# Kernel optimization log

Measured on AMD Instinct MI355X. Metric: run time of the kernel, lower is better.

Reference implementation:

```python
import jax, jax.numpy as jnp
import numpy as np

N_HEADS = 8
NUM_GROUPS = 2
HEAD_DIM = 256
ROPE_DIM = 64
IDIM = 2048
GROUP_SIZE = N_HEADS // NUM_GROUPS  # 4
ODIM = N_HEADS * HEAD_DIM           # 2048
N_KV = NUM_GROUPS * HEAD_DIM        # 512
EPS = 1e-6


def rms_norm(x, gamma):
    # normalize over last dim (head_dim)
    var = jnp.mean(jnp.square(x), axis=-1, keepdims=True)
    return x * jax.lax.rsqrt(var + EPS) * gamma


def rotate_half(x):
    x1, x2 = jnp.split(x, 2, axis=-1)
    return jnp.concatenate([-x2, x1], axis=-1)


def apply_rope(x, cos, sin):
    # x: (..., L, rope_dim); cos/sin: (L, rope_dim) broadcast
    return x * cos + rotate_half(x) * sin


def setup_inputs() -> dict:
    key = jax.random.key(0)
    ks = jax.random.split(key, 10)
    B, L = 1, 4096
    x = jax.random.normal(ks[0], (B, L, IDIM), dtype=jnp.float32)
    # rope angles
    inv_freq = 1.0 / (10000.0 ** (jnp.arange(0, ROPE_DIM, 2, dtype=jnp.float32) / ROPE_DIM))
    t = jnp.arange(L, dtype=jnp.float32)
    freqs = jnp.outer(t, inv_freq)                      # (L, rope_dim/2)
    emb = jnp.concatenate([freqs, freqs], axis=-1)      # (L, rope_dim)
    cos = jnp.cos(emb)
    sin = jnp.sin(emb)
    # causal mask: True = masked out
    mask = jnp.triu(jnp.ones((L, L), dtype=bool), k=1)
    s = 0.02
    wq = jax.random.normal(ks[1], (IDIM, ODIM * 2), dtype=jnp.float32) * s
    wk = jax.random.normal(ks[2], (IDIM, N_KV), dtype=jnp.float32) * s
    wv = jax.random.normal(ks[3], (IDIM, N_KV), dtype=jnp.float32) * s
    wo = jax.random.normal(ks[4], (ODIM, IDIM), dtype=jnp.float32) * s
    q_gamma = jnp.ones((HEAD_DIM,), dtype=jnp.float32)
    k_gamma = jnp.ones((HEAD_DIM,), dtype=jnp.float32)
    return {"x": x, "cos": cos, "sin": sin, "mask": mask,
            "wq": wq, "wk": wk, "wv": wv, "wo": wo,
            "q_gamma": q_gamma, "k_gamma": k_gamma}


def reference(x, cos, sin, mask, wq, wk, wv, wo, q_gamma, k_gamma):
    b, L, _ = x.shape
    scale = HEAD_DIM ** -0.5
    # query + output gate
    q_raw = (x @ wq).reshape(b, L, N_HEADS, 2 * HEAD_DIM)
    q, gate = jnp.split(q_raw, 2, axis=-1)
    gate = gate.reshape(b, L, ODIM)
    q = jnp.transpose(q, (0, 2, 1, 3))                  # (b, h, L, d)
    # grouped K/V
    k = (x @ wk).reshape(b, L, NUM_GROUPS, HEAD_DIM).transpose(0, 2, 1, 3)  # (b, g, L, d)
    v = (x @ wv).reshape(b, L, NUM_GROUPS, HEAD_DIM).transpose(0, 2, 1, 3)
    # QK RMSNorm
    q = rms_norm(q, q_gamma)
    k = rms_norm(k, k_gamma)
    # partial RoPE on first ROPE_DIM dims
    q = jnp.concatenate([apply_rope(q[..., :ROPE_DIM], cos, sin), q[..., ROPE_DIM:]], axis=-1)
    k = jnp.concatenate([apply_rope(k[..., :ROPE_DIM], cos, sin), k[..., ROPE_DIM:]], axis=-1)
    # GQA without materializing repeated K/V: head h = g*GROUP_SIZE + s
    qg = q.reshape(b, NUM_GROUPS, GROUP_SIZE, L, HEAD_DIM)
    dots = jnp.einsum('bgsid,bgjd->bgsij', qg, k) * scale
    dots = jnp.where(mask, -jnp.inf, dots)
    attn = jax.nn.softmax(dots, axis=-1)
    out = jnp.einsum('bgsij,bgjd->bgsid', attn, v)      # (b, g, gs, L, d)
    out = out.reshape(b, N_HEADS, L, HEAD_DIM).transpose(0, 2, 1, 3).reshape(b, L, ODIM)
    out = out * jax.nn.sigmoid(gate)
    return out @ wo
```

## Files before the change

### kernel.cpp

```cpp
#include <hip/hip_runtime.h>
#include <hip/hip_bf16.h>
#include <math.h>

typedef __bf16 bf16_t;
typedef __bf16 bf16x4 __attribute__((ext_vector_type(4)));
typedef __bf16 bf16x8 __attribute__((ext_vector_type(8)));
typedef float  f32x4  __attribute__((ext_vector_type(4)));
typedef float  f32x16 __attribute__((ext_vector_type(16)));
typedef unsigned int u32x4 __attribute__((ext_vector_type(4)));

typedef const __attribute__((address_space(1))) void* gas_ptr;
typedef __attribute__((address_space(3))) void* las_ptr;

#define RD_ 64
#define QKVS 5120

__global__ __launch_bounds__(256) void cvt_f32_bf16(const float* __restrict__ in,
                                                    bf16_t* __restrict__ out) {
  int i = (blockIdx.x * 256 + threadIdx.x) * 4;
  float4 v = *(const float4*)&in[i];
  bf16x4 w;
  w[0] = (bf16_t)v.x; w[1] = (bf16_t)v.y; w[2] = (bf16_t)v.z; w[3] = (bf16_t)v.w;
  *(bf16x4*)&out[i] = w;
}

__global__ __launch_bounds__(256) void transpose_cvt(const float* __restrict__ in,
                                                     bf16_t* __restrict__ out,
                                                     int R, int C) {
  __shared__ bf16_t t[32][33];
  int tx = threadIdx.x & 31, ty = threadIdx.x >> 5;
  int c0 = blockIdx.x * 32, r0 = blockIdx.y * 32;
#pragma unroll
  for (int i = 0; i < 4; i++)
    t[ty + 8 * i][tx] = (bf16_t)in[(size_t)(r0 + ty + 8 * i) * C + c0 + tx];
  __syncthreads();
#pragma unroll
  for (int i = 0; i < 4; i++)
    out[(size_t)(c0 + ty + 8 * i) * R + r0 + tx] = t[tx][ty + 8 * i];
}

__global__ __launch_bounds__(256) void transpose_bf16(const bf16_t* __restrict__ in,
                                                      bf16_t* __restrict__ out,
                                                      int R, int C) {
  __shared__ bf16_t t[32][33];
  int tx = threadIdx.x & 31, ty = threadIdx.x >> 5;
  int c0 = blockIdx.x * 32, r0 = blockIdx.y * 32;
#pragma unroll
  for (int i = 0; i < 4; i++)
    t[ty + 8 * i][tx] = in[(size_t)(r0 + ty + 8 * i) * C + c0 + tx];
  __syncthreads();
#pragma unroll
  for (int i = 0; i < 4; i++)
    out[(size_t)(c0 + ty + 8 * i) * R + r0 + tx] = t[tx][ty + 8 * i];
}

#define GM 128
#define GN 128
#define GK 32

template <typename OutT>
__global__ __launch_bounds__(256) void gemm_bt(const bf16_t* __restrict__ A,
                                               const bf16_t* __restrict__ Bt,
                                               OutT* __restrict__ C,
                                               int M, int N, int K) {
  __shared__ bf16_t As[GM * GK];
  __shared__ bf16_t Bs[GN * GK];
  int tid  = threadIdx.x;
  int lane = tid & 63, wave = tid >> 6;
  int wm = (wave & 1) * 64, wn = (wave >> 1) * 64;
  int bm = blockIdx.x * GM, bn = blockIdx.y * GN;
  int qd = lane >> 4, lr = lane & 15;

  f32x4 acc[4][4] = {};

  int srow = wave * 16 + (lane >> 2);
  int scol = (lane & 3) * 8;
  const bf16_t* ga0 = A  + (size_t)(bm + srow) * K + scol;
  const bf16_t* ga1 = A  + (size_t)(bm + 64 + srow) * K + scol;
  const bf16_t* gb0 = Bt + (size_t)(bn + srow) * K + scol;
  const bf16_t* gb1 = Bt + (size_t)(bn + 64 + srow) * K + scol;
  las_ptr lA0 = (las_ptr)(As + wave * 512);
  las_ptr lA1 = (las_ptr)(As + 64 * 32 + wave * 512);
  las_ptr lB0 = (las_ptr)(Bs + wave * 512);
  las_ptr lB1 = (las_ptr)(Bs + 64 * 32 + wave * 512);

  for (int k0 = 0; k0 < K; k0 += GK) {
    __syncthreads();
    __builtin_amdgcn_global_load_lds((gas_ptr)(ga0 + k0), lA0, 16, 0, 0);
    __builtin_amdgcn_global_load_lds((gas_ptr)(ga1 + k0), lA1, 16, 0, 0);
    __builtin_amdgcn_global_load_lds((gas_ptr)(gb0 + k0), lB0, 16, 0, 0);
    __builtin_amdgcn_global_load_lds((gas_ptr)(gb1 + k0), lB1, 16, 0, 0);
    __syncthreads();

    bf16x8 af[4], bfr[4];
#pragma unroll
    for (int t = 0; t < 4; t++) {
      af[t]  = *(const bf16x8*)&As[(wm + t * 16 + lr) * GK + qd * 8];
      bfr[t] = *(const bf16x8*)&Bs[(wn + t * 16 + lr) * GK + qd * 8];
    }
#pragma unroll
    for (int mt = 0; mt < 4; mt++)
#pragma unroll
      for (int nt = 0; nt < 4; nt++)
        acc[mt][nt] = __builtin_amdgcn_mfma_f32_16x16x32_bf16(af[mt], bfr[nt], acc[mt][nt], 0, 0, 0);
  }

#pragma unroll
  for (int mt = 0; mt < 4; mt++) {
    int rb = bm + wm + mt * 16 + qd * 4;
#pragma unroll
    for (int nt = 0; nt < 4; nt++) {
      int cc = bn + wn + nt * 16 + lr;
#pragma unroll
      for (int r = 0; r < 4; r++)
        C[(size_t)(rb + r) * N + cc] = (OutT)acc[mt][nt][r];
    }
  }
}

template <int NHEADS, int HSTRIDE, int RSTRIDE>
__global__ __launch_bounds__(256) void norm_rope(const bf16_t* __restrict__ in,
                                                 bf16_t* __restrict__ out,
                                                 const float* __restrict__ cosv,
                                                 const float* __restrict__ sinv,
                                                 const float* __restrict__ gamma) {
  int lane = threadIdx.x & 63;
  int idx  = blockIdx.x * 4 + (threadIdx.x >> 6);
  int l = idx / NHEADS, h = idx % NHEADS;
  size_t base = (size_t)l * RSTRIDE + (size_t)h * HSTRIDE;
  int d0 = lane * 4;

  bf16x4 raw = *(const bf16x4*)&in[base + d0];
  float x[4];
#pragma unroll
  for (int i = 0; i < 4; i++) x[i] = (float)raw[i];
  float ss = x[0] * x[0] + x[1] * x[1] + x[2] * x[2] + x[3] * x[3];
#pragma unroll
  for (int off = 32; off >= 1; off >>= 1) ss += __shfl_xor(ss, off);
  float inv = 1.0f / sqrtf(ss * (1.0f / 256.0f) + 1e-6f);

  float4 gr = *(const float4*)&gamma[d0];
  float n[4];
#pragma unroll
  for (int i = 0; i < 4; i++) n[i] = x[i] * inv * ((const float*)&gr)[i];

  float p[4];
#pragma unroll
  for (int i = 0; i < 4; i++) p[i] = __shfl_xor(n[i], 8);
  float o[4];
#pragma unroll
  for (int i = 0; i < 4; i++) o[i] = n[i];
  if (lane < 16) {
    float4 cr = *(const float4*)&cosv[(size_t)l * RD_ + d0];
    float4 sr = *(const float4*)&sinv[(size_t)l * RD_ + d0];
#pragma unroll
    for (int i = 0; i < 4; i++) {
      float rh = (lane < 8) ? -p[i] : p[i];
      o[i] = n[i] * ((const float*)&cr)[i] + rh * ((const float*)&sr)[i];
    }
  }
  bf16x4 w;
#pragma unroll
  for (int i = 0; i < 4; i++) w[i] = (bf16_t)o[i];
  *(bf16x4*)&out[base + d0] = w;
}

__global__ __launch_bounds__(256, 2) void attn_mfma(const bf16_t* __restrict__ qraw,
                                                    const bf16_t* __restrict__ kn,
                                                    const bf16_t* __restrict__ vt,
                                                    bf16_t* __restrict__ outg,
                                                    float* __restrict__ pO,
                                                    float* __restrict__ pL) {
  __shared__ __align__(16) bf16_t ks[2][32 * 256];
  __shared__ __align__(16) bf16_t vs[2][256 * 32];
  int tid = threadIdx.x, lane = tid & 63, wave = tid >> 6;
  int m = lane & 31, hi = lane >> 5;
  int b = blockIdx.x;
  int h = b & 7, g = h >> 2, i = b >> 3;

  int qb, tile0, nt; bool fin = false;
  if (i < 16) { qb = 31 - i; tile0 = 0; nt = 64; }
  else {
    int u = (i - 16) >> 1;
    if (((i - 16) & 1) == 0) { qb = 15 - u; tile0 = 0; nt = 4 * qb + 4; fin = true; }
    else                     { qb = 31 - u; tile0 = 64; nt = 4 * qb + 4 - 64; }
  }

  int qrow0 = qb * 128 + wave * 32;
  int qg = qrow0 + m;
  int qmax = qrow0 + 31;

  bf16x8 qf[16];
  {
    const bf16_t* qp = qraw + (size_t)(qrow0 + m) * QKVS + h * 512 + hi * 8;
#pragma unroll
    for (int kb = 0; kb < 16; kb++) qf[kb] = *(const bf16x8*)(qp + kb * 16);
  }

  int xk = m & 7;
  int kofs[4];
#pragma unroll
  for (int bb = 0; bb < 4; bb++)
    kofs[bb] = m * 256 + ((bb ^ (xk >> 1)) * 2 + (hi ^ (xk & 1))) * 8;
  int swv = (m ^ (m >> 2)) & 3;
  int vofs[2];
#pragma unroll
  for (int k2 = 0; k2 < 2; k2++)
    vofs[k2] = m * 32 + (((k2 * 2 + hi) ^ swv) * 8);

  const bf16_t* ksrc = kn + (size_t)(wave * 2 + hi) * QKVS + g * 256
                          + (size_t)((m ^ ((wave * 2 + hi) & 7)) * 8);
  int swsrc = ((lane >> 2) ^ (lane >> 4)) & 3;
  const bf16_t* vsrc = vt + (size_t)(g * 256 + wave * 16 + (lane >> 2)) * 4096
                          + (size_t)(((lane & 3) ^ swsrc) * 8);

  f32x16 o[8] = {};
  float ladd = 0.0f;

#define STAGE(buf, j0)                                                                      \
  do {                                                                                      \
    bf16_t* kd = &ks[buf][0] + wave * 512;                                                  \
    bf16_t* vd = &vs[buf][0] + wave * 512;                                                  \
    _Pragma("unroll")                                                                       \
    for (int s = 0; s < 4; s++)                                                             \
      __builtin_amdgcn_global_load_lds((gas_ptr)(ksrc + (size_t)(j0) * QKVS + s * 8 * QKVS),\
                                       (las_ptr)(kd + s * 2048), 16, 0, 0);                 \
    _Pragma("unroll")                                                                       \
    for (int s = 0; s < 4; s++)                                                             \
      __builtin_amdgcn_global_load_lds((gas_ptr)(vsrc + (size_t)(j0) + (size_t)s * 262144), \
                                       (las_ptr)(vd + s * 2048), 16, 0, 0);                 \
  } while (0)

  STAGE(0, tile0 * 32);
  asm volatile("s_waitcnt vmcnt(0)" ::: "memory");
  __syncthreads();

  for (int t = 0; t < nt; t++) {
    int cur = t & 1;
    if (t + 1 < nt) STAGE(cur ^ 1, (tile0 + t + 1) * 32);
    int j0 = (tile0 + t) * 32;
    if (j0 <= qmax) {
      f32x16 sa = {};
#pragma unroll
      for (int kb = 0; kb < 16; kb++) {
        bf16x8 kf = *(const bf16x8*)&ks[cur][kofs[kb & 3] + (kb >> 2) * 64];
        sa = __builtin_amdgcn_mfma_f32_32x32x16_bf16(kf, qf[kb], sa, 0, 0, 0);
      }

      bool diag = (j0 + 31 > qrow0);
#pragma unroll
      for (int k2 = 0; k2 < 2; k2++) {
        float pp[8];
#pragma unroll
        for (int r = 0; r < 8; r++) {
          int rr = k2 * 8 + r;
          float e = __expf(sa[rr] * 0.0625f - 20.0f);
          if (diag) {
            int jr = j0 + (rr & 3) + 8 * (rr >> 2) + 4 * hi;
            if (jr > qg) e = 0.0f;
          }
          pp[r] = e;
        }
        unsigned a0, b0, a1, b1;
        asm("v_cvt_pk_bf16_f32 %0, %1, %2" : "=v"(a0) : "v"(pp[0]), "v"(pp[1]));
        asm("v_cvt_pk_bf16_f32 %0, %1, %2" : "=v"(b0) : "v"(pp[4]), "v"(pp[5]));
        asm("v_cvt_pk_bf16_f32 %0, %1, %2" : "=v"(a1) : "v"(pp[2]), "v"(pp[3]));
        asm("v_cvt_pk_bf16_f32 %0, %1, %2" : "=v"(b1) : "v"(pp[6]), "v"(pp[7]));
        asm("v_permlane32_swap_b32 %0, %1" : "+v"(a0), "+v"(b0));
        asm("v_permlane32_swap_b32 %0, %1" : "+v"(a1), "+v"(b1));
        u32x4 uw = {a0, a1, b0, b1};
        bf16x8 pa = __builtin_bit_cast(bf16x8, uw);
#pragma unroll
        for (int ii = 0; ii < 4; ii++) {
          unsigned w = uw[ii];
          ladd += __builtin_bit_cast(float, w << 16);
          ladd += __builtin_bit_cast(float, w & 0xffff0000u);
        }
#pragma unroll
        for (int dt = 0; dt < 8; dt++) {
          bf16x8 vf = *(const bf16x8*)&vs[cur][vofs[k2] + dt * 1024];
          o[dt] = __builtin_amdgcn_mfma_f32_32x32x16_bf16(pa, vf, o[dt], 0, 0, 0);
        }
      }
    }
    asm volatile("s_waitcnt vmcnt(0)" ::: "memory");
    __syncthreads();
  }
#undef STAGE

  float lo = ladd + __shfl_xor(ladd, 32);

  if (fin) {
    float linv[16];
#pragma unroll
    for (int r = 0; r < 16; r++)
      linv[r] = 1.0f / __shfl(lo, (r & 3) + 8 * (r >> 2) + 4 * hi, 64);
    const bf16_t* gb = qraw + (size_t)qrow0 * QKVS + h * 512 + 256;
#pragma unroll
    for (int dt = 0; dt < 8; dt++)
#pragma unroll
      for (int r = 0; r < 16; r++) {
        int q = (r & 3) + 8 * (r >> 2) + 4 * hi;
        int d = dt * 32 + m;
        float gt = (float)gb[(size_t)q * QKVS + d];
        float sg = 1.0f / (1.0f + __expf(-gt));
        outg[(size_t)(qrow0 + q) * 2048 + h * 256 + d] = (bf16_t)(o[dt][r] * linv[r] * sg);
      }
  } else {
    int sidx = (h * 16 + (qb - 16)) * 2 + (tile0 ? 1 : 0);
    if (hi == 0) pL[(size_t)sidx * 128 + wave * 32 + m] = lo;
    size_t ob = (size_t)sidx * 32768 + (size_t)(wave * 32) * 256;
#pragma unroll
    for (int dt = 0; dt < 8; dt++)
#pragma unroll
      for (int r = 0; r < 16; r++) {
        int q = (r & 3) + 8 * (r >> 2) + 4 * hi;
        pO[ob + (size_t)q * 256 + dt * 32 + m] = o[dt][r];
      }
  }
}

__global__ __launch_bounds__(256) void attn_combine(const float* __restrict__ pO,
                                                    const float* __restrict__ pL,
                                                    const bf16_t* __restrict__ qkv,
                                                    bf16_t* __restrict__ outg) {
  int b = blockIdx.x;
  int h = b & 7, qbc = 16 + (b >> 3);
  int tid = threadIdx.x;
  int r = tid >> 1, half = tid & 1;
  int row = qbc * 128 + r;
  size_t sA = ((size_t)h * 16 + (qbc - 16)) * 2;

  float lsum = pL[sA * 128 + r] + pL[(sA + 1) * 128 + r];
  float linv = 1.0f / lsum;

  const bf16_t* gb = qkv + (size_t)row * QKVS + h * 512 + 256 + half * 128;
  bf16_t* op = outg + (size_t)row * 2048 + h * 256 + half * 128;
  size_t p0 = sA * 32768 + (size_t)r * 256 + half * 128;
  size_t p1 = p0 + 32768;
#pragma unroll 4
  for (int d = 0; d < 128; d += 4) {
    float4 a = *(const float4*)&pO[p0 + d];
    float4 c = *(const float4*)&pO[p1 + d];
    bf16x4 gr = *(const bf16x4*)&gb[d];
    float vv[4] = {a.x + c.x, a.y + c.y, a.z + c.z, a.w + c.w};
    bf16x4 w;
#pragma unroll
    for (int i = 0; i < 4; i++) {
      float sg = 1.0f / (1.0f + __expf(-(float)gr[i]));
      w[i] = (bf16_t)(vv[i] * linv * sg);
    }
    *(bf16x4*)&op[d] = w;
  }
}

extern "C" void kernel_launch(void* const* d_in, const int* in_sizes, int n_in,
                              void* d_out, int out_size, void* d_ws, size_t ws_size,
                              hipStream_t stream) {
  const float* x    = (const float*)d_in[0];
  const float* cosv = (const float*)d_in[1];
  const float* sinv = (const float*)d_in[2];
  const float* wq   = (const float*)d_in[4];
  const float* wk   = (const float*)d_in[5];
  const float* wv   = (const float*)d_in[6];
  const float* wo   = (const float*)d_in[7];
  const float* qg   = (const float*)d_in[8];
  const float* kg   = (const float*)d_in[9];
  float* outp = (float*)d_out;

  char* ws = (char*)d_ws;
  size_t off = 0;
  auto alloc = [&](size_t bytes) { char* p = ws + off; off += (bytes + 255) & ~255ull; return p; };

  bf16_t* qkv_raw = (bf16_t*)alloc((size_t)4096 * QKVS * 2);
  bf16_t* v_t     = (bf16_t*)alloc((size_t)512 * 4096 * 2);
  bf16_t* attn_g  = (bf16_t*)alloc((size_t)4096 * 2048 * 2);
  bf16_t* woT     = (bf16_t*)alloc((size_t)2048 * 2048 * 2);

  size_t scratch0 = off;
  bf16_t* x_bf  = (bf16_t*)alloc((size_t)4096 * 2048 * 2);
  bf16_t* wqkvT = (bf16_t*)alloc((size_t)QKVS * 2048 * 2);

  float* pO = (float*)(ws + scratch0);
  size_t poEnd = scratch0 + (size_t)256 * 32768 * 4;
  if (off < poEnd) off = (poEnd + 255) & ~255ull;
  float* pL = (float*)alloc((size_t)256 * 128 * 4);

  dim3 blk(256);
  cvt_f32_bf16<<<8192, blk, 0, stream>>>(x, x_bf);

  transpose_cvt<<<dim3(4096 / 32, 2048 / 32), blk, 0, stream>>>(wq, wqkvT, 2048, 4096);
  transpose_cvt<<<dim3(512 / 32, 2048 / 32), blk, 0, stream>>>(wk, wqkvT + (size_t)4096 * 2048, 2048, 512);
  transpose_cvt<<<dim3(512 / 32, 2048 / 32), blk, 0, stream>>>(wv, wqkvT + (size_t)4608 * 2048, 2048, 512);
  transpose_cvt<<<dim3(2048 / 32, 2048 / 32), blk, 0, stream>>>(wo, woT, 2048, 2048);

  gemm_bt<bf16_t><<<dim3(4096 / 128, QKVS / 128), blk, 0, stream>>>(x_bf, wqkvT, qkv_raw, 4096, QKVS, 2048);

  norm_rope<8, 512, QKVS><<<4096 * 8 / 4, blk, 0, stream>>>(qkv_raw, qkv_raw, cosv, sinv, qg);
  norm_rope<2, 256, QKVS><<<4096 * 2 / 4, blk, 0, stream>>>(qkv_raw + 4096, qkv_raw + 4096, cosv, sinv, kg);

  transpose_bf16<<<dim3(512 / 32, 4096 / 32), blk, 0, stream>>>(qkv_raw + 4608, v_t, 4096, QKVS);

  attn_mfma<<<dim3(384), blk, 0, stream>>>(qkv_raw, qkv_raw + 4096, v_t, attn_g, pO, pL);
  attn_combine<<<dim3(128), blk, 0, stream>>>(pO, pL, qkv_raw, attn_g);

  gemm_bt<float><<<dim3(4096 / 128, 2048 / 128), blk, 0, stream>>>(attn_g, woT, outp, 4096, 2048, 2048);
}
```

Before: 517.1 us.

## Process 64 query rows per wave with two waves per attention block

The attention kernel now launches 128 threads (2 waves) per block instead of 256, and each wave handles two 32-row query sub-tiles. Every K fragment read from LDS feeds two score MFMAs, which halves K LDS reads per unit of work. Staging loops are reorganized so two waves load the full K/V tiles. In exchange, per-wave register pressure roughly doubles (two sets of Q fragments and output accumulators), occupancy drops with launch bounds (128,1), and each block has fewer waves to hide latency.

After: 739.0 us. +42.9%, slower.

```diff
diff --git a/kernel.cpp b/kernel.cpp
--- a/kernel.cpp
+++ b/kernel.cpp
@@ -165,7 +165,7 @@
   *(bf16x4*)&out[base + d0] = w;
 }
 
-__global__ __launch_bounds__(256, 2) void attn_mfma(const bf16_t* __restrict__ qraw,
+__global__ __launch_bounds__(128, 1) void attn_mfma(const bf16_t* __restrict__ qraw,
                                                     const bf16_t* __restrict__ kn,
                                                     const bf16_t* __restrict__ vt,
                                                     bf16_t* __restrict__ outg,
@@ -186,15 +186,18 @@
     else                     { qb = 31 - u; tile0 = 64; nt = 4 * qb + 4 - 64; }
   }
 
-  int qrow0 = qb * 128 + wave * 32;
-  int qg = qrow0 + m;
-  int qmax = qrow0 + 31;
-
-  bf16x8 qf[16];
+  int qrow0 = qb * 128 + wave * 64;
+  int qmaxw = qrow0 + 63;
+
+  bf16x8 qf0[16], qf1[16];
   {
-    const bf16_t* qp = qraw + (size_t)(qrow0 + m) * QKVS + h * 512 + hi * 8;
-#pragma unroll
-    for (int kb = 0; kb < 16; kb++) qf[kb] = *(const bf16x8*)(qp + kb * 16);
+    const bf16_t* qp0 = qraw + (size_t)(qrow0 + m) * QKVS + h * 512 + hi * 8;
+    const bf16_t* qp1 = qp0 + (size_t)32 * QKVS;
+#pragma unroll
+    for (int kb = 0; kb < 16; kb++) {
+      qf0[kb] = *(const bf16x8*)(qp0 + kb * 16);
+      qf1[kb] = *(const bf16x8*)(qp1 + kb * 16);
+    }
   }
 
   int xk = m & 7;
@@ -208,27 +211,29 @@
   for (int k2 = 0; k2 < 2; k2++)
     vofs[k2] = m * 32 + (((k2 * 2 + hi) ^ swv) * 8);
 
-  const bf16_t* ksrc = kn + (size_t)(wave * 2 + hi) * QKVS + g * 256
-                          + (size_t)((m ^ ((wave * 2 + hi) & 7)) * 8);
+  int krA = wave * 2 + hi, krB = wave * 2 + 4 + hi;
+  const bf16_t* ksrcA = kn + (size_t)krA * QKVS + g * 256 + (size_t)((m ^ krA) * 8);
+  const bf16_t* ksrcB = kn + (size_t)krB * QKVS + g * 256 + (size_t)((m ^ krB) * 8);
   int swsrc = ((lane >> 2) ^ (lane >> 4)) & 3;
   const bf16_t* vsrc = vt + (size_t)(g * 256 + wave * 16 + (lane >> 2)) * 4096
                           + (size_t)(((lane & 3) ^ swsrc) * 8);
 
-  f32x16 o[8] = {};
-  float ladd = 0.0f;
-
-#define STAGE(buf, j0)                                                                      \
-  do {                                                                                      \
-    bf16_t* kd = &ks[buf][0] + wave * 512;                                                  \
-    bf16_t* vd = &vs[buf][0] + wave * 512;                                                  \
-    _Pragma("unroll")                                                                       \
-    for (int s = 0; s < 4; s++)                                                             \
-      __builtin_amdgcn_global_load_lds((gas_ptr)(ksrc + (size_t)(j0) * QKVS + s * 8 * QKVS),\
-                                       (las_ptr)(kd + s * 2048), 16, 0, 0);                 \
-    _Pragma("unroll")                                                                       \
-    for (int s = 0; s < 4; s++)                                                             \
-      __builtin_amdgcn_global_load_lds((gas_ptr)(vsrc + (size_t)(j0) + (size_t)s * 262144), \
-                                       (las_ptr)(vd + s * 2048), 16, 0, 0);                 \
+  f32x16 o0[8] = {}, o1[8] = {};
+  float ladd0 = 0.0f, ladd1 = 0.0f;
+
+#define STAGE(buf, j0)                                                                        \
+  do {                                                                                        \
+    _Pragma("unroll")                                                                         \
+    for (int s = 0; s < 4; s++) {                                                             \
+      __builtin_amdgcn_global_load_lds((gas_ptr)(ksrcA + (size_t)(j0) * QKVS + s * 8 * QKVS), \
+                                       (las_ptr)(&ks[buf][0] + (wave + 4 * s) * 512), 16, 0, 0);\
+      __builtin_amdgcn_global_load_lds((gas_ptr)(ksrcB + (size_t)(j0) * QKVS + s * 8 * QKVS), \
+                                       (las_ptr)(&ks[buf][0] + (wave + 2 + 4 * s) * 512), 16, 0, 0);\
+    }                                                                                         \
+    _Pragma("unroll")                                                                         \
+    for (int s = 0; s < 8; s++)                                                               \
+      __builtin_amdgcn_global_load_lds((gas_ptr)(vsrc + (size_t)(j0) + (size_t)s * 131072),   \
+                                       (las_ptr)(&vs[buf][0] + (wave + 2 * s) * 512), 16, 0, 0);\
   } while (0)
 
   STAGE(0, tile0 * 32);
@@ -239,47 +244,57 @@
     int cur = t & 1;
     if (t + 1 < nt) STAGE(cur ^ 1, (tile0 + t + 1) * 32);
     int j0 = (tile0 + t) * 32;
-    if (j0 <= qmax) {
-      f32x16 sa = {};
+    if (j0 <= qmaxw) {
+      f32x16 sa0 = {}, sa1 = {};
 #pragma unroll
       for (int kb = 0; kb < 16; kb++) {
         bf16x8 kf = *(const bf16x8*)&ks[cur][kofs[kb & 3] + (kb >> 2) * 64];
-        sa = __builtin_amdgcn_mfma_f32_32x32x16_bf16(kf, qf[kb], sa, 0, 0, 0);
+        sa0 = __builtin_amdgcn_mfma_f32_32x32x16_bf16(kf, qf0[kb], sa0, 0, 0, 0);
+        sa1 = __builtin_amdgcn_mfma_f32_32x32x16_bf16(kf, qf1[kb], sa1, 0, 0, 0);
       }
 
-      bool diag = (j0 + 31 > qrow0);
-#pragma unroll
-      for (int k2 = 0; k2 < 2; k2++) {
-        float pp[8];
-#pragma unroll
-        for (int r = 0; r < 8; r++) {
-          int rr = k2 * 8 + r;
-          float e = __expf(sa[rr] * 0.0625f - 20.0f);
-          if (diag) {
-            int jr = j0 + (rr & 3) + 8 * (rr >> 2) + 4 * hi;
-            if (jr > qg) e = 0.0f;
+#pragma unroll
+      for (int st = 0; st < 2; st++) {
+        int qs0 = qrow0 + st * 32;
+        if (j0 > qs0 + 31) continue;
+        const f32x16& sa = st ? sa1 : sa0;
+        f32x16* o = st ? o1 : o0;
+        float& ladd = st ? ladd1 : ladd0;
+        int qg = qs0 + m;
+        bool diag = (j0 + 31 > qs0);
+#pragma unroll
+        for (int k2 = 0; k2 < 2; k2++) {
+          float pp[8];
+#pragma unroll
+          for (int r = 0; r < 8; r++) {
+            int rr = k2 * 8 + r;
+            float e = __expf(sa[rr] * 0.0625f - 20.0f);
+            if (diag) {
+              int jr = j0 + (rr & 3) + 8 * (rr >> 2) + 4 * hi;
+              if (jr > qg) e = 0.0f;
+            }
+            pp[r] = e;
           }
-          pp[r] = e;
-        }
-        unsigned a0, b0, a1, b1;
-        asm("v_cvt_pk_bf16_f32 %0, %1, %2" : "=v"(a0) : "v"(pp[0]), "v"(pp[1]));
-        asm("v_cvt_pk_bf16_f32 %0, %1, %2" : "=v"(b0) : "v"(pp[4]), "v"(pp[5]));
-        asm("v_cvt_pk_bf16_f32 %0, %1, %2" : "=v"(a1) : "v"(pp[2]), "v"(pp[3]));
-        asm("v_cvt_pk_bf16_f32 %0, %1, %2" : "=v"(b1) : "v"(pp[6]), "v"(pp[7]));
-        asm("v_permlane32_swap_b32 %0, %1" : "+v"(a0), "+v"(b0));
-        asm("v_permlane32_swap_b32 %0, %1" : "+v"(a1), "+v"(b1));
-        u32x4 uw = {a0, a1, b0, b1};
-        bf16x8 pa = __builtin_bit_cast(bf16x8, uw);
-#pragma unroll
-        for (int ii = 0; ii < 4; ii++) {
-          unsigned w = uw[ii];
-          ladd += __builtin_bit_cast(float, w << 16);
-          ladd += __builtin_bit_cast(float, w & 0xffff0000u);
-        }
-#pragma unroll
-        for (int dt = 0; dt < 8; dt++) {
-          bf16x8 vf = *(const bf16x8*)&vs[cur][vofs[k2] + dt * 1024];
-          o[dt] = __builtin_amdgcn_mfma_f32_32x32x16_bf16(pa, vf, o[dt], 0, 0, 0);
+          unsigned a0, b0, a1, b1;
+          asm("v_cvt_pk_bf16_f32 %0, %1, %2" : "=v"(a0) : "v"(pp[0]), "v"(pp[1]));
+          asm("v_cvt_pk_bf16_f32 %0, %1, %2" : "=v"(b0) : "v"(pp[4]), "v"(pp[5]));
+          asm("v_cvt_pk_bf16_f32 %0, %1, %2" : "=v"(a1) : "v"(pp[2]), "v"(pp[3]));
+          asm("v_cvt_pk_bf16_f32 %0, %1, %2" : "=v"(b1) : "v"(pp[6]), "v"(pp[7]));
+          asm("v_permlane32_swap_b32 %0, %1" : "+v"(a0), "+v"(b0));
+          asm("v_permlane32_swap_b32 %0, %1" : "+v"(a1), "+v"(b1));
+          u32x4 uw = {a0, a1, b0, b1};
+          bf16x8 pa = __builtin_bit_cast(bf16x8, uw);
+#pragma unroll
+          for (int ii = 0; ii < 4; ii++) {
+            unsigned w = uw[ii];
+            ladd += __builtin_bit_cast(float, w << 16);
+            ladd += __builtin_bit_cast(float, w & 0xffff0000u);
+          }
+#pragma unroll
+          for (int dt = 0; dt < 8; dt++) {
+            bf16x8 vf = *(const bf16x8*)&vs[cur][vofs[k2] + dt * 1024];
+            o[dt] = __builtin_amdgcn_mfma_f32_32x32x16_bf16(pa, vf, o[dt], 0, 0, 0);
+          }
         }
       }
     }
@@ -288,35 +303,48 @@
   }
 #undef STAGE
 
-  float lo = ladd + __shfl_xor(ladd, 32);
+  float lo0 = ladd0 + __shfl_xor(ladd0, 32);
+  float lo1 = ladd1 + __shfl_xor(ladd1, 32);
 
   if (fin) {
-    float linv[16];
-#pragma unroll
-    for (int r = 0; r < 16; r++)
-      linv[r] = 1.0f / __shfl(lo, (r & 3) + 8 * (r >> 2) + 4 * hi, 64);
-    const bf16_t* gb = qraw + (size_t)qrow0 * QKVS + h * 512 + 256;
-#pragma unroll
-    for (int dt = 0; dt < 8; dt++)
-#pragma unroll
-      for (int r = 0; r < 16; r++) {
-        int q = (r & 3) + 8 * (r >> 2) + 4 * hi;
-        int d = dt * 32 + m;
-        float gt = (float)gb[(size_t)q * QKVS + d];
-        float sg = 1.0f / (1.0f + __expf(-gt));
-        outg[(size_t)(qrow0 + q) * 2048 + h * 256 + d] = (bf16_t)(o[dt][r] * linv[r] * sg);
-      }
+#pragma unroll
+    for (int st = 0; st < 2; st++) {
+      float lo = st ? lo1 : lo0;
+      const f32x16* o = st ? o1 : o0;
+      int qs0 = qrow0 + st * 32;
+      float linv[16];
+#pragma unroll
+      for (int r = 0; r < 16; r++)
+        linv[r] = 1.0f / __shfl(lo, (r & 3) + 8 * (r >> 2) + 4 * hi, 64);
+      const bf16_t* gb = qraw + (size_t)qs0 * QKVS + h * 512 + 256;
+#pragma unroll
+      for (int dt = 0; dt < 8; dt++)
+#pragma unroll
+        for (int r = 0; r < 16; r++) {
+          int q = (r & 3) + 8 * (r >> 2) + 4 * hi;
+          int d = dt * 32 + m;
+          float gt = (float)gb[(size_t)q * QKVS + d];
+          float sg = 1.0f / (1.0f + __expf(-gt));
+          outg[(size_t)(qs0 + q) * 2048 + h * 256 + d] = (bf16_t)(o[dt][r] * linv[r] * sg);
+        }
+    }
   } else {
     int sidx = (h * 16 + (qb - 16)) * 2 + (tile0 ? 1 : 0);
-    if (hi == 0) pL[(size_t)sidx * 128 + wave * 32 + m] = lo;
-    size_t ob = (size_t)sidx * 32768 + (size_t)(wave * 32) * 256;
-#pragma unroll
-    for (int dt = 0; dt < 8; dt++)
-#pragma unroll
-      for (int r = 0; r < 16; r++) {
-        int q = (r & 3) + 8 * (r >> 2) + 4 * hi;
-        pO[ob + (size_t)q * 256 + dt * 32 + m] = o[dt][r];
-      }
+#pragma unroll
+    for (int st = 0; st < 2; st++) {
+      float lo = st ? lo1 : lo0;
+      const f32x16* o = st ? o1 : o0;
+      int rbase = wave * 64 + st * 32;
+      if (hi == 0) pL[(size_t)sidx * 128 + rbase + m] = lo;
+      size_t ob = (size_t)sidx * 32768 + (size_t)rbase * 256;
+#pragma unroll
+      for (int dt = 0; dt < 8; dt++)
+#pragma unroll
+        for (int r = 0; r < 16; r++) {
+          int q = (r & 3) + 8 * (r >> 2) + 4 * hi;
+          pO[ob + (size_t)q * 256 + dt * 32 + m] = o[dt][r];
+        }
+    }
   }
 }
 
@@ -401,7 +429,7 @@
 
   transpose_bf16<<<dim3(512 / 32, 4096 / 32), blk, 0, stream>>>(qkv_raw + 4608, v_t, 4096, QKVS);
 
-  attn_mfma<<<dim3(384), blk, 0, stream>>>(qkv_raw, qkv_raw + 4096, v_t, attn_g, pO, pL);
+  attn_mfma<<<dim3(384), dim3(128), 0, stream>>>(qkv_raw, qkv_raw + 4096, v_t, attn_g, pO, pL);
   attn_combine<<<dim3(128), blk, 0, stream>>>(pO, pL, qkv_raw, attn_g);
 
   gemm_bt<float><<<dim3(4096 / 128, 2048 / 128), blk, 0, stream>>>(attn_g, woT, outp, 4096, 2048, 2048);
```

## Split attention KV range into up to four chunks per query block

Applied to the files above, without the earlier changes.

Rebalances the causal attention work: query blocks are split into 1-4 KV chunks depending on their length, raising the grid from 384 to 640 blocks. The combine kernel now sums a variable number of partials, and the partial buffers grow accordingly. It also raises wave priority during the MFMA/softmax section and folds the exp scale into a single fma feeding exp2. The goal is better CU load balance and less tail time, at the cost of more partial-sum traffic and a larger combine pass.

Result: slower. 562.2 us (+8.7%).

```diff
diff --git a/kernel.cpp b/kernel.cpp
--- a/kernel.cpp
+++ b/kernel.cpp
@@ -176,15 +176,19 @@
   int tid = threadIdx.x, lane = tid & 63, wave = tid >> 6;
   int m = lane & 31, hi = lane >> 5;
   int b = blockIdx.x;
-  int h = b & 7, g = h >> 2, i = b >> 3;
-
-  int qb, tile0, nt; bool fin = false;
-  if (i < 16) { qb = 31 - i; tile0 = 0; nt = 64; }
-  else {
-    int u = (i - 16) >> 1;
-    if (((i - 16) & 1) == 0) { qb = 15 - u; tile0 = 0; nt = 4 * qb + 4; fin = true; }
-    else                     { qb = 31 - u; tile0 = 64; nt = 4 * qb + 4 - 64; }
-  }
+  int h = b & 7, g = h >> 2, bp = b >> 3;
+
+  int qb, c, C;
+  if (bp < 32)      { qb = 31 - (bp >> 2);       c = bp & 3;        C = 4; }
+  else if (bp < 56) { int t = bp - 32; qb = 23 - t / 3; c = t % 3;  C = 3; }
+  else if (bp < 72) { int t = bp - 56; qb = 15 - (t >> 1); c = t & 1; C = 2; }
+  else              { qb = 7 - (bp - 72);        c = 0;             C = 1; }
+  bool fin = (C == 1);
+
+  int ntf  = 4 * qb + 4;
+  int base = ntf / C, rem = ntf % C;
+  int tile0 = c * base + (c < rem ? c : rem);
+  int nt = base + (c < rem ? 1 : 0);
 
   int qrow0 = qb * 128 + wave * 32;
   int qg = qrow0 + m;
@@ -240,6 +244,7 @@
     if (t + 1 < nt) STAGE(cur ^ 1, (tile0 + t + 1) * 32);
     int j0 = (tile0 + t) * 32;
     if (j0 <= qmax) {
+      __builtin_amdgcn_s_setprio(1);
       f32x16 sa = {};
 #pragma unroll
       for (int kb = 0; kb < 16; kb++) {
@@ -254,7 +259,7 @@
 #pragma unroll
         for (int r = 0; r < 8; r++) {
           int rr = k2 * 8 + r;
-          float e = __expf(sa[rr] * 0.0625f - 20.0f);
+          float e = exp2f(__builtin_fmaf(sa[rr], 0.09016844f, -28.8539008f));
           if (diag) {
             int jr = j0 + (rr & 3) + 8 * (rr >> 2) + 4 * hi;
             if (jr > qg) e = 0.0f;
@@ -282,6 +287,7 @@
           o[dt] = __builtin_amdgcn_mfma_f32_32x32x16_bf16(pa, vf, o[dt], 0, 0, 0);
         }
       }
+      __builtin_amdgcn_s_setprio(0);
     }
     asm volatile("s_waitcnt vmcnt(0)" ::: "memory");
     __syncthreads();
@@ -307,7 +313,11 @@
         outg[(size_t)(qrow0 + q) * 2048 + h * 256 + d] = (bf16_t)(o[dt][r] * linv[r] * sg);
       }
   } else {
-    int sidx = (h * 16 + (qb - 16)) * 2 + (tile0 ? 1 : 0);
+    int slot;
+    if (qb >= 24)      slot = 40 + 4 * (qb - 24) + c;
+    else if (qb >= 16) slot = 16 + 3 * (qb - 16) + c;
+    else               slot = 2 * (qb - 8) + c;
+    int sidx = h * 72 + slot;
     if (hi == 0) pL[(size_t)sidx * 128 + wave * 32 + m] = lo;
     size_t ob = (size_t)sidx * 32768 + (size_t)(wave * 32) * 256;
 #pragma unroll
@@ -325,25 +335,33 @@
                                                     const bf16_t* __restrict__ qkv,
                                                     bf16_t* __restrict__ outg) {
   int b = blockIdx.x;
-  int h = b & 7, qbc = 16 + (b >> 3);
+  int h = b & 7, qbc = 8 + (b >> 3);
+  int C, slot0;
+  if (qbc >= 24)      { C = 4; slot0 = 40 + 4 * (qbc - 24); }
+  else if (qbc >= 16) { C = 3; slot0 = 16 + 3 * (qbc - 16); }
+  else                { C = 2; slot0 = 2 * (qbc - 8); }
+  size_t sA = (size_t)h * 72 + slot0;
+
   int tid = threadIdx.x;
   int r = tid >> 1, half = tid & 1;
   int row = qbc * 128 + r;
-  size_t sA = ((size_t)h * 16 + (qbc - 16)) * 2;
-
-  float lsum = pL[sA * 128 + r] + pL[(sA + 1) * 128 + r];
+
+  float lsum = 0.0f;
+  for (int cc = 0; cc < C; cc++) lsum += pL[(sA + cc) * 128 + r];
   float linv = 1.0f / lsum;
 
   const bf16_t* gb = qkv + (size_t)row * QKVS + h * 512 + 256 + half * 128;
   bf16_t* op = outg + (size_t)row * 2048 + h * 256 + half * 128;
-  size_t p0 = sA * 32768 + (size_t)r * 256 + half * 128;
-  size_t p1 = p0 + 32768;
+  size_t pbase = sA * 32768 + (size_t)r * 256 + half * 128;
 #pragma unroll 4
   for (int d = 0; d < 128; d += 4) {
-    float4 a = *(const float4*)&pO[p0 + d];
-    float4 c = *(const float4*)&pO[p1 + d];
+    float a0 = 0, a1 = 0, a2 = 0, a3 = 0;
+    for (int cc = 0; cc < C; cc++) {
+      float4 v = *(const float4*)&pO[pbase + (size_t)cc * 32768 + d];
+      a0 += v.x; a1 += v.y; a2 += v.z; a3 += v.w;
+    }
+    float vv[4] = {a0, a1, a2, a3};
     bf16x4 gr = *(const bf16x4*)&gb[d];
-    float vv[4] = {a.x + c.x, a.y + c.y, a.z + c.z, a.w + c.w};
     bf16x4 w;
 #pragma unroll
     for (int i = 0; i < 4; i++) {
@@ -382,9 +400,9 @@
   bf16_t* wqkvT = (bf16_t*)alloc((size_t)QKVS * 2048 * 2);
 
   float* pO = (float*)(ws + scratch0);
-  size_t poEnd = scratch0 + (size_t)256 * 32768 * 4;
+  size_t poEnd = scratch0 + (size_t)576 * 32768 * 4;
   if (off < poEnd) off = (poEnd + 255) & ~255ull;
-  float* pL = (float*)alloc((size_t)256 * 128 * 4);
+  float* pL = (float*)alloc((size_t)576 * 128 * 4);
 
   dim3 blk(256);
   cvt_f32_bf16<<<8192, blk, 0, stream>>>(x, x_bf);
@@ -401,8 +419,8 @@
 
   transpose_bf16<<<dim3(512 / 32, 4096 / 32), blk, 0, stream>>>(qkv_raw + 4608, v_t, 4096, QKVS);
 
-  attn_mfma<<<dim3(384), blk, 0, stream>>>(qkv_raw, qkv_raw + 4096, v_t, attn_g, pO, pL);
-  attn_combine<<<dim3(128), blk, 0, stream>>>(pO, pL, qkv_raw, attn_g);
+  attn_mfma<<<dim3(640), blk, 0, stream>>>(qkv_raw, qkv_raw + 4096, v_t, attn_g, pO, pL);
+  attn_combine<<<dim3(192), blk, 0, stream>>>(pO, pL, qkv_raw, attn_g);
 
   gemm_bt<float><<<dim3(4096 / 128, 2048 / 128), blk, 0, stream>>>(attn_g, woT, outp, 4096, 2048, 2048);
 }
```
